# Kernel tuning notes

Measured on AMD Instinct MI355X. Metric: run time of the kernel, lower is better.

The kernel has to match this reference:

```python
import jax, jax.numpy as jnp
import numpy as np

H = 128
NC, NM, ND = 50000, 30000, 10000
E_CM, E_MD, E_CD = 800000, 400000, 800000


def setup_inputs() -> dict:
    key = jax.random.key(0)
    ks = jax.random.split(key, 20)
    nrm = lambda k, s: jax.random.normal(k, s, dtype=jnp.float32)
    ri = lambda k, n, hi: jax.random.randint(k, (n,), 0, hi, dtype=jnp.int32)
    scale = 1.0 / np.sqrt(H)
    return {
        'x_c': nrm(ks[0], (NC, H)),
        'x_m': nrm(ks[1], (NM, H)),
        'x_d': nrm(ks[2], (ND, H)),
        'src_cm': ri(ks[3], E_CM, NC), 'dst_cm': ri(ks[4], E_CM, NM),
        'src_md': ri(ks[5], E_MD, NM), 'dst_md': ri(ks[6], E_MD, ND),
        'src_cd': ri(ks[7], E_CD, NC), 'dst_cd': ri(ks[8], E_CD, ND),
        'src_mc': ri(ks[9], E_CM, NM), 'dst_mc': ri(ks[10], E_CM, NC),
        'src_dm': ri(ks[11], E_MD, ND), 'dst_dm': ri(ks[12], E_MD, NM),
        'src_dc': ri(ks[13], E_CD, ND), 'dst_dc': ri(ks[14], E_CD, NC),
        'Wl': nrm(ks[15], (4, 6, H, H)) * scale,  # lin_l per (layer, relation)
        'Wr': nrm(ks[16], (4, 6, H, H)) * scale,  # lin_r (root) per (layer, relation)
        'b': nrm(ks[17], (4, 6, H)) * scale,      # lin_l bias
    }


def _segment_mean(feat, seg, n):
    s = jax.ops.segment_sum(feat, seg, num_segments=n)
    cnt = jax.ops.segment_sum(jnp.ones((seg.shape[0], 1), feat.dtype), seg, num_segments=n)
    return s / jnp.maximum(cnt, 1.0)


def reference(x_c, x_m, x_d,
              src_cm, dst_cm, src_md, dst_md, src_cd, dst_cd,
              src_mc, dst_mc, src_dm, dst_dm, src_dc, dst_dc,
              Wl, Wr, b):
    # relation order: (c->m), (m->d), (c->d), (m->c), (d->m), (d->c)
    rels = [(src_cm, dst_cm, 'c', 'm', NM), (src_md, dst_md, 'm', 'd', ND),
            (src_cd, dst_cd, 'c', 'd', ND), (src_mc, dst_mc, 'm', 'c', NC),
            (src_dm, dst_dm, 'd', 'm', NM), (src_dc, dst_dc, 'd', 'c', NC)]

    def layer(h, l):
        outs = []
        for r, (s, dst, st, dt, nd) in enumerate(rels):
            agg = _segment_mean(h[st][s], dst, nd)          # gather + scatter-mean
            outs.append(agg @ Wl[l, r] + h[dt] @ Wr[l, r] + b[l, r])
        # HeteroConv aggr='mean': each dst type receives exactly 2 relations
        return {'c': (outs[3] + outs[5]) * 0.5,
                'm': (outs[0] + outs[4]) * 0.5,
                'd': (outs[1] + outs[2]) * 0.5}

    h = {'c': x_c, 'm': x_m, 'd': x_d}
    for l in range(3):
        h = layer(h, l)
        h = {k: jax.nn.relu(v) for k, v in h.items()}  # dropout is identity in eval
    h = layer(h, 3)

    def l2n(v):
        return v / jnp.maximum(jnp.linalg.norm(v, axis=1, keepdims=True), 1e-12)

    return (l2n(h['c']), l2n(h['m']), l2n(h['d']))
```

## Files before the change

### kernel.cpp

```cpp
#include <hip/hip_runtime.h>
#include <hip/hip_bf16.h>


#define NC_N 50000
#define NM_N 30000
#define ND_N 10000
#define NTOT 90000
#define H    128

typedef __attribute__((ext_vector_type(8))) short short8;
typedef __attribute__((ext_vector_type(4))) float f32x4;

__device__ __forceinline__ ushort f2bf(float f) {
    uint u = __float_as_uint(f);
    return (ushort)((u + 0x7fffu + ((u >> 16) & 1u)) >> 16);
}
__device__ __forceinline__ float bflo(uint v) { return __uint_as_float(v << 16); }
__device__ __forceinline__ float bfhi(uint v) { return __uint_as_float(v & 0xffff0000u); }

#define ACHUNK 2048

struct BuildArgs {
    const int* dstp[6];
    const int* srcp[6];
    int ablockBase[7];
    int binBase[7];
    int E[6];
    int offsBase[6];
    int csrBase[6];
    int nDst[6];
    int shift[6];
};

__global__ __launch_bounds__(256)
void bincount_k(BuildArgs a, int* __restrict__ binCnt) {
    __shared__ int hist[128];
    int blk = blockIdx.x, r = 0;
    #pragma unroll
    for (int k = 1; k <= 5; ++k) if (blk >= a.ablockBase[k]) r = k;
    const int i0 = (blk - a.ablockBase[r]) * ACHUNK;
    const int E = a.E[r], sh = a.shift[r];
    const int tid = threadIdx.x;
    if (tid < 128) hist[tid] = 0;
    __syncthreads();
    #pragma unroll
    for (int k = 0; k < 8; ++k) {
        int i = i0 + k * 256 + tid;
        if (i < E) atomicAdd(&hist[a.dstp[r][i] >> sh], 1);
    }
    __syncthreads();
    if (tid < 128 && hist[tid] > 0)
        atomicAdd(&binCnt[a.binBase[r] + tid], hist[tid]);
}

__global__ void binscan_k(const int* __restrict__ binCnt, int* __restrict__ binOffs,
                          int* __restrict__ binCur, int totBins) {
    __shared__ int buf[1024];
    int tid = threadIdx.x;
    int v = (tid < totBins) ? binCnt[tid] : 0;
    buf[tid] = v;
    __syncthreads();
    #pragma unroll
    for (int off = 1; off < 1024; off <<= 1) {
        int t = (tid >= off) ? buf[tid - off] : 0;
        __syncthreads();
        buf[tid] += t;
        __syncthreads();
    }
    if (tid < totBins) {
        int excl = buf[tid] - v;
        binOffs[tid] = excl;
        binCur[tid]  = excl;
        if (tid == totBins - 1) binOffs[totBins] = buf[tid];
    }
}

__global__ __launch_bounds__(256)
void binscat_k(BuildArgs a, int* __restrict__ binCur, int2* __restrict__ staging) {
    __shared__ int hist[128], hbase[128], hcur[128];
    int blk = blockIdx.x, r = 0;
    #pragma unroll
    for (int k = 1; k <= 5; ++k) if (blk >= a.ablockBase[k]) r = k;
    const int i0 = (blk - a.ablockBase[r]) * ACHUNK;
    const int E = a.E[r], sh = a.shift[r];
    const int tid = threadIdx.x;
    if (tid < 128) { hist[tid] = 0; hcur[tid] = 0; }
    __syncthreads();
    int d[8], s[8], bn[8];
    bool ok[8];
    #pragma unroll
    for (int k = 0; k < 8; ++k) {
        int i = i0 + k * 256 + tid;
        ok[k] = (i < E);
        if (ok[k]) {
            d[k] = a.dstp[r][i];
            s[k] = a.srcp[r][i];
            bn[k] = d[k] >> sh;
            atomicAdd(&hist[bn[k]], 1);
        }
    }
    __syncthreads();
    if (tid < 128 && hist[tid] > 0)
        hbase[tid] = atomicAdd(&binCur[a.binBase[r] + tid], hist[tid]);
    __syncthreads();
    #pragma unroll
    for (int k = 0; k < 8; ++k) {
        if (ok[k]) {
            int lr = atomicAdd(&hcur[bn[k]], 1);
            staging[hbase[bn[k]] + lr] = make_int2(s[k], d[k]);
        }
    }
}

__global__ __launch_bounds__(256)
void binplace2_k(BuildArgs a, const int* __restrict__ binOffs,
                 const int2* __restrict__ staging,
                 int* __restrict__ offsAll, int* __restrict__ csr) {
    __shared__ int cnt[512];
    __shared__ int sbuf[512];
    int g = blockIdx.x, r = 0;
    #pragma unroll
    for (int k = 1; k <= 5; ++k) if (g >= a.binBase[k]) r = k;
    const int b = g - a.binBase[r];
    const int sh = a.shift[r];
    const int dlo = b << sh;
    const int dhi = min(dlo + (1 << sh), a.nDst[r]);
    const int nd = dhi - dlo;
    const int tid = threadIdx.x;
    const int i0 = tid, i1 = tid + 256;
    cnt[i0] = 0; cnt[i1] = 0;
    __syncthreads();
    const int eBase = binOffs[g];
    const int eEnd  = binOffs[g + 1];
    for (int i = eBase + tid; i < eEnd; i += 256)
        atomicAdd(&cnt[staging[i].y - dlo], 1);
    __syncthreads();
    sbuf[i0] = cnt[i0]; sbuf[i1] = cnt[i1];
    __syncthreads();
    #pragma unroll
    for (int off = 1; off < 512; off <<= 1) {
        int t0 = (i0 >= off) ? sbuf[i0 - off] : 0;
        int t1 = (i1 >= off) ? sbuf[i1 - off] : 0;
        __syncthreads();
        sbuf[i0] += t0; sbuf[i1] += t1;
        __syncthreads();
    }
    const int eRel = eBase - a.csrBase[r];
    int e0 = sbuf[i0] - cnt[i0];
    int e1 = sbuf[i1] - cnt[i1];
    if (i0 < nd) { offsAll[a.offsBase[r] + dlo + i0] = eRel + e0; cnt[i0] = eBase + e0; }
    if (i1 < nd) { offsAll[a.offsBase[r] + dlo + i1] = eRel + e1; cnt[i1] = eBase + e1; }
    if (tid == 0 && dhi == a.nDst[r])
        offsAll[a.offsBase[r] + a.nDst[r]] = eRel + (eEnd - eBase);
    __syncthreads();
    for (int i = eBase + tid; i < eEnd; i += 256) {
        int2 p = staging[i];
        int pos = atomicAdd(&cnt[p.y - dlo], 1);
        csr[pos] = p.x;
    }
}

__global__ void prep_w_k(const float* __restrict__ Wl, const float* __restrict__ Wr,
                         const float* __restrict__ b,
                         ushort* __restrict__ WlT, ushort* __restrict__ WsumT,
                         float* __restrict__ bsum) {
    const int rA[3] = {3, 0, 1}, rB[3] = {5, 4, 2};
    int blk = blockIdx.x, tid = threadIdx.x;
    int nr = tid >> 1;
    int k0 = (tid & 1) * 64;
    if (blk < 24) {
        const float* src = Wl + (size_t)blk * 16384;
        ushort* dst = WlT + (size_t)blk * 16384;
        for (int k = k0; k < k0 + 64; ++k)
            dst[nr * 128 + k] = f2bf(src[k * 128 + nr]);
    } else {
        int lt = blk - 24, l = lt / 3, t = lt % 3;
        const float* sA = Wr + (size_t)(l * 6 + rA[t]) * 16384;
        const float* sB = Wr + (size_t)(l * 6 + rB[t]) * 16384;
        ushort* dst = WsumT + (size_t)lt * 16384;
        for (int k = k0; k < k0 + 64; ++k)
            dst[nr * 128 + k] = f2bf(sA[k * 128 + nr] + sB[k * 128 + nr]);
        if (tid < 128)
            bsum[lt * 128 + tid] = b[(l * 6 + rA[t]) * 128 + tid] +
                                   b[(l * 6 + rB[t]) * 128 + tid];
    }
}

__global__ void cvt_x_k(const float* __restrict__ xc, const float* __restrict__ xm,
                        const float* __restrict__ xd, ushort* __restrict__ h) {
    int i = blockIdx.x * 256 + threadIdx.x;
    const int tot = NTOT * H / 8;
    if (i >= tot) return;
    size_t base = (size_t)i * 8;
    int row = (int)(base >> 7);
    const float* src; size_t local;
    if (row < NC_N) { src = xc; local = base; }
    else if (row < NC_N + NM_N) { src = xm; local = base - (size_t)NC_N * H; }
    else { src = xd; local = base - (size_t)(NC_N + NM_N) * H; }
    float4 v0 = *(const float4*)(src + local);
    float4 v1 = *(const float4*)(src + local + 4);
    uint4 o;
    o.x = (uint)f2bf(v0.x) | ((uint)f2bf(v0.y) << 16);
    o.y = (uint)f2bf(v0.z) | ((uint)f2bf(v0.w) << 16);
    o.z = (uint)f2bf(v1.x) | ((uint)f2bf(v1.y) << 16);
    o.w = (uint)f2bf(v1.z) | ((uint)f2bf(v1.w) << 16);
    *(uint4*)(h + base) = o;
}

struct AggArgs {
    const ushort* src[6];
    const int* offs[6];
    const int* csr[6];
    ushort* out[6];
    int n[3];
    int blockBase[4];
    int halfBlocks[3];
};

__global__ __launch_bounds__(256)
void agg_all_k(AggArgs ga) {
    const int b = blockIdx.x;
    const int t = (b >= ga.blockBase[2]) ? 2 : (b >= ga.blockBase[1]) ? 1 : 0;
    const int local = b - ga.blockBase[t];
    const int isB = (local >= ga.halfBlocks[t]) ? 1 : 0;
    const int ridx = 2 * t + isB;
    const uint2* __restrict__ src = (const uint2*)ga.src[ridx];
    const int* __restrict__ offs  = ga.offs[ridx];
    const int* __restrict__ csr   = ga.csr[ridx];
    uint2* __restrict__ out       = (uint2*)ga.out[ridx];
    const int n = ga.n[t];
    const int w = (local - isB * ga.halfBlocks[t]) * 4 + (int)(threadIdx.x >> 6);
    if (w >= n) return;
    const int lane = threadIdx.x & 63;
    const int half = lane >> 5;
    const int lh   = lane & 31;
    const int s = offs[w], e = offs[w + 1];

    float a0 = 0.f, a1 = 0.f, a2 = 0.f, a3 = 0.f;
    int j = s;
    for (; j + 16 <= e; j += 16) {
        int i0 = csr[j + 0  + half], i1 = csr[j + 2  + half];
        int i2 = csr[j + 4  + half], i3 = csr[j + 6  + half];
        int i4 = csr[j + 8  + half], i5 = csr[j + 10 + half];
        int i6 = csr[j + 12 + half], i7 = csr[j + 14 + half];
        uint2 v0 = src[(size_t)i0 * 32 + lh];
        uint2 v1 = src[(size_t)i1 * 32 + lh];
        uint2 v2 = src[(size_t)i2 * 32 + lh];
        uint2 v3 = src[(size_t)i3 * 32 + lh];
        uint2 v4 = src[(size_t)i4 * 32 + lh];
        uint2 v5 = src[(size_t)i5 * 32 + lh];
        uint2 v6 = src[(size_t)i6 * 32 + lh];
        uint2 v7 = src[(size_t)i7 * 32 + lh];
        a0 += bflo(v0.x) + bflo(v1.x) + bflo(v2.x) + bflo(v3.x)
            + bflo(v4.x) + bflo(v5.x) + bflo(v6.x) + bflo(v7.x);
        a1 += bfhi(v0.x) + bfhi(v1.x) + bfhi(v2.x) + bfhi(v3.x)
            + bfhi(v4.x) + bfhi(v5.x) + bfhi(v6.x) + bfhi(v7.x);
        a2 += bflo(v0.y) + bflo(v1.y) + bflo(v2.y) + bflo(v3.y)
            + bflo(v4.y) + bflo(v5.y) + bflo(v6.y) + bflo(v7.y);
        a3 += bfhi(v0.y) + bfhi(v1.y) + bfhi(v2.y) + bfhi(v3.y)
            + bfhi(v4.y) + bfhi(v5.y) + bfhi(v6.y) + bfhi(v7.y);
    }
    for (; j + 2 <= e; j += 2) {
        int i0 = csr[j + half];
        uint2 v = src[(size_t)i0 * 32 + lh];
        a0 += bflo(v.x); a1 += bfhi(v.x); a2 += bflo(v.y); a3 += bfhi(v.y);
    }
    if (j < e && half == 0) {
        int i0 = csr[j];
        uint2 v = src[(size_t)i0 * 32 + lh];
        a0 += bflo(v.x); a1 += bfhi(v.x); a2 += bflo(v.y); a3 += bfhi(v.y);
    }
    a0 += __shfl_xor(a0, 32);
    a1 += __shfl_xor(a1, 32);
    a2 += __shfl_xor(a2, 32);
    a3 += __shfl_xor(a3, 32);
    if (half == 0) {
        const float inv = 1.0f / fmaxf((float)(e - s), 1.0f);
        uint2 o;
        o.x = (uint)f2bf(a0 * inv) | ((uint)f2bf(a1 * inv) << 16);
        o.y = (uint)f2bf(a2 * inv) | ((uint)f2bf(a3 * inv) << 16);
        out[(size_t)w * 32 + lh] = o;
    }
}

struct GemmArgs {
    const ushort* A1[3]; const ushort* W1[3];
    const ushort* A2[3]; const ushort* W2[3];
    const ushort* A3[3]; const ushort* W3[3];
    const float* bias[3];
    void* out[3];
    int n[3];
    int blockBase[4];
    int mode;
};

__global__ __launch_bounds__(256)
void gemm_all_k(GemmArgs ga) {
    __shared__ ushort As[128][40];
    __shared__ ushort Bs[128][40];
    const int b = blockIdx.x;
    const int t = (b >= ga.blockBase[2]) ? 2 : (b >= ga.blockBase[1]) ? 1 : 0;
    const int tid  = threadIdx.x;
    const int wave = tid >> 6, lane = tid & 63;
    const int lr = lane & 15, lk = lane >> 4;
    const int row0 = (b - ga.blockBase[t]) * 128;
    const int n = ga.n[t];

    f32x4 acc[2][8];
    #pragma unroll
    for (int i = 0; i < 2; ++i)
        #pragma unroll
        for (int j = 0; j < 8; ++j) acc[i][j] = (f32x4)0.f;

    const ushort* Ap[3] = {ga.A1[t], ga.A2[t], ga.A3[t]};
    const ushort* Wp[3] = {ga.W1[t], ga.W2[t], ga.W3[t]};

    const int rs = tid >> 2;
    const int kb = (tid & 3) * 8;

    for (int term = 0; term < 3; ++term) {
        const ushort* A = Ap[term];
        const ushort* W = Wp[term];
        #pragma unroll 1
        for (int k0 = 0; k0 < 128; k0 += 32) {
            #pragma unroll
            for (int p = 0; p < 2; ++p) {
                int rr = rs + p * 64;
                int gr = row0 + rr;
                short8 av = (short8)0;
                if (gr < n) av = *(const short8*)(A + (size_t)gr * 128 + k0 + kb);
                *(short8*)&As[rr][kb] = av;
                short8 wv = *(const short8*)(W + (size_t)rr * 128 + k0 + kb);
                *(short8*)&Bs[rr][kb] = wv;
            }
            __syncthreads();
            short8 af0 = *(const short8*)&As[wave * 32 + lr][lk * 8];
            short8 af1 = *(const short8*)&As[wave * 32 + 16 + lr][lk * 8];
            #pragma unroll
            for (int nt = 0; nt < 8; ++nt) {
                short8 bf = *(const short8*)&Bs[nt * 16 + lr][lk * 8];
                acc[0][nt] = __builtin_amdgcn_mfma_f32_16x16x32_bf16(af0, bf, acc[0][nt], 0, 0, 0);
                acc[1][nt] = __builtin_amdgcn_mfma_f32_16x16x32_bf16(af1, bf, acc[1][nt], 0, 0, 0);
            }
            __syncthreads();
        }
    }
    float bv[8];
    #pragma unroll
    for (int nt = 0; nt < 8; ++nt) bv[nt] = ga.bias[t][nt * 16 + lr];

    if (ga.mode == 0) {
        ushort* outp = (ushort*)ga.out[t];
        #pragma unroll
        for (int mt = 0; mt < 2; ++mt) {
            #pragma unroll
            for (int nt = 0; nt < 8; ++nt) {
                int col = nt * 16 + lr;
                #pragma unroll
                for (int r = 0; r < 4; ++r) {
                    int row = row0 + wave * 32 + mt * 16 + lk * 4 + r;
                    if (row < n) {
                        float v = fmaxf(0.5f * (acc[mt][nt][r] + bv[nt]), 0.f);
                        outp[(size_t)row * 128 + col] = f2bf(v);
                    }
                }
            }
        }
    } else {
        float* outp = (float*)ga.out[t];
        #pragma unroll
        for (int mt = 0; mt < 2; ++mt) {
            #pragma unroll
            for (int r = 0; r < 4; ++r) {
                float v[8]; float ss = 0.f;
                #pragma unroll
                for (int nt = 0; nt < 8; ++nt) {
                    v[nt] = 0.5f * (acc[mt][nt][r] + bv[nt]);
                    ss += v[nt] * v[nt];
                }
                ss += __shfl_xor(ss, 1);
                ss += __shfl_xor(ss, 2);
                ss += __shfl_xor(ss, 4);
                ss += __shfl_xor(ss, 8);
                float scale = 1.0f / fmaxf(sqrtf(ss), 1e-12f);
                int row = row0 + wave * 32 + mt * 16 + lk * 4 + r;
                if (row < n) {
                    #pragma unroll
                    for (int nt = 0; nt < 8; ++nt)
                        outp[(size_t)row * 128 + nt * 16 + lr] = v[nt] * scale;
                }
            }
        }
    }
}

extern "C" void kernel_launch(void* const* d_in, const int* in_sizes, int n_in,
                              void* d_out, int out_size, void* d_ws, size_t ws_size,
                              hipStream_t stream) {
    const float* x[3] = {(const float*)d_in[0], (const float*)d_in[1], (const float*)d_in[2]};
    const int* srcp[6] = {(const int*)d_in[3], (const int*)d_in[5], (const int*)d_in[7],
                          (const int*)d_in[9], (const int*)d_in[11], (const int*)d_in[13]};
    const int* dstp[6] = {(const int*)d_in[4], (const int*)d_in[6], (const int*)d_in[8],
                          (const int*)d_in[10], (const int*)d_in[12], (const int*)d_in[14]};
    const float* Wl = (const float*)d_in[15];
    const float* Wr = (const float*)d_in[16];
    const float* b  = (const float*)d_in[17];
    float* outp = (float*)d_out;

    const int nNode[3]   = {NC_N, NM_N, ND_N};
    const int E[6]       = {800000, 400000, 800000, 800000, 400000, 800000};
    const int nDst[6]    = {NM_N, ND_N, ND_N, NC_N, NM_N, NC_N};
    const int shiftR[6]  = {8, 7, 7, 9, 8, 9};
    const int srcType[6] = {0, 1, 0, 1, 2, 2};
    const int relA[3] = {3, 0, 1}, relB[3] = {5, 4, 2};

    char* p = (char*)d_ws;
    auto alloc = [&](size_t bytes) -> char* {
        char* r = p; p += (bytes + 255) & ~(size_t)255; return r;
    };
    ushort* hA    = (ushort*)alloc((size_t)NTOT * H * 2);
    ushort* hB    = (ushort*)alloc((size_t)NTOT * H * 2);
    ushort* aggA[3], * aggB[3];
    for (int t = 0; t < 3; ++t) {
        aggA[t] = (ushort*)alloc((size_t)nNode[t] * H * 2);
        aggB[t] = (ushort*)alloc((size_t)nNode[t] * H * 2);
    }
    ushort* WlT   = (ushort*)alloc((size_t)24 * H * H * 2);
    ushort* WsumT = (ushort*)alloc((size_t)12 * H * H * 2);
    float*  bsum  = (float*)alloc((size_t)12 * H * 4);
    int*    offs  = (int*)alloc((size_t)180006 * 4);
    int*    csr   = (int*)alloc((size_t)4000000 * 4);
    int*    binCnt  = (int*)alloc((size_t)1024 * 4);
    int*    binOffs = (int*)alloc((size_t)1025 * 4);
    int*    binCur  = (int*)alloc((size_t)1024 * 4);
    int2*   staging = (int2*)hA;

    BuildArgs ba;
    int totBins = 0;
    { int ob = 0, cb = 0, ab = 0, gb = 0;
      for (int r = 0; r < 6; ++r) {
          ba.dstp[r] = dstp[r]; ba.srcp[r] = srcp[r];
          ba.E[r] = E[r]; ba.nDst[r] = nDst[r]; ba.shift[r] = shiftR[r];
          ba.ablockBase[r] = ab; ab += (E[r] + ACHUNK - 1) / ACHUNK;
          ba.binBase[r]    = gb; gb += (nDst[r] + (1 << shiftR[r]) - 1) >> shiftR[r];
          ba.offsBase[r] = ob; ob += nDst[r] + 1;
          ba.csrBase[r]  = cb; cb += E[r];
      }
      ba.ablockBase[6] = ab; ba.binBase[6] = gb;
      totBins = gb; }

    hipMemsetAsync(binCnt, 0, totBins * 4, stream);
    bincount_k<<<ba.ablockBase[6], 256, 0, stream>>>(ba, binCnt);
    binscan_k<<<1, 1024, 0, stream>>>(binCnt, binOffs, binCur, totBins);
    binscat_k<<<ba.ablockBase[6], 256, 0, stream>>>(ba, binCur, staging);
    binplace2_k<<<totBins, 256, 0, stream>>>(ba, binOffs, staging, offs, csr);

    prep_w_k<<<36, 256, 0, stream>>>(Wl, Wr, b, WlT, WsumT, bsum);
    cvt_x_k<<<(NTOT * H / 8 + 255) / 256, 256, 0, stream>>>(x[0], x[1], x[2], hA);

    const size_t tOff[3] = {0, (size_t)NC_N * H, (size_t)(NC_N + NM_N) * H};
    ushort* hb[2] = {hA, hB};

    int cur = 0;
    for (int l = 0; l < 4; ++l) {
        ushort* hsrc = hb[cur];
        ushort* hdst = hb[cur ^ 1];

        AggArgs aa;
        int aggBlocks = 0;
        for (int t = 0; t < 3; ++t) {
            int rA = relA[t], rB = relB[t];
            aa.src[2 * t]     = hsrc + tOff[srcType[rA]];
            aa.offs[2 * t]    = offs + ba.offsBase[rA];
            aa.csr[2 * t]     = csr + ba.csrBase[rA];
            aa.out[2 * t]     = aggA[t];
            aa.src[2 * t + 1] = hsrc + tOff[srcType[rB]];
            aa.offs[2 * t + 1]= offs + ba.offsBase[rB];
            aa.csr[2 * t + 1] = csr + ba.csrBase[rB];
            aa.out[2 * t + 1] = aggB[t];
            aa.n[t] = nNode[t];
            aa.halfBlocks[t] = (nNode[t] + 3) / 4;
            aa.blockBase[t] = aggBlocks;
            aggBlocks += 2 * aa.halfBlocks[t];
        }
        aa.blockBase[3] = aggBlocks;
        agg_all_k<<<aggBlocks, 256, 0, stream>>>(aa);

        GemmArgs ga;
        int gemmBlocks = 0;
        for (int t = 0; t < 3; ++t) {
            int rA = relA[t], rB = relB[t];
            ga.A1[t] = aggA[t]; ga.W1[t] = WlT + (size_t)(l * 6 + rA) * H * H;
            ga.A2[t] = aggB[t]; ga.W2[t] = WlT + (size_t)(l * 6 + rB) * H * H;
            ga.A3[t] = hsrc + tOff[t];
            ga.W3[t] = WsumT + (size_t)(l * 3 + t) * H * H;
            ga.bias[t] = bsum + (size_t)(l * 3 + t) * H;
            ga.out[t] = (l < 3) ? (void*)(hdst + tOff[t]) : (void*)(outp + tOff[t]);
            ga.n[t] = nNode[t];
            ga.blockBase[t] = gemmBlocks;
            gemmBlocks += (nNode[t] + 127) / 128;
        }
        ga.blockBase[3] = gemmBlocks;
        ga.mode = (l < 3) ? 0 : 1;
        gemm_all_k<<<gemmBlocks, 256, 0, stream>>>(ga);

        cur ^= 1;
    }
}
```

Measured before the change: 877.0 us.

## Pad CSR adjacency rows to multiples of 16 with zero-row sentinel

The CSR build now pads each destination's neighbor list to a multiple of 16 entries, filling the extra slots with an index pointing at an all-zero row appended to the feature buffers. The aggregation kernel then runs only its fully unrolled 16-wide gather loop, with no tail loops. This removes the low-parallelism remainder iterations and their divergence. In exchange it adds redundant gathers of the zero row, a larger CSR array, and a second scan in the build.

```diff
diff --git a/kernel.cpp b/kernel.cpp
--- a/kernel.cpp
+++ b/kernel.cpp
@@ -7,6 +7,7 @@
 #define ND_N 10000
 #define NTOT 90000
 #define H    128
+#define PADG 16
 
 typedef __attribute__((ext_vector_type(8))) short short8;
 typedef __attribute__((ext_vector_type(4))) float f32x4;
@@ -30,6 +31,8 @@
     int csrBase[6];
     int nDst[6];
     int shift[6];
+    int padBase[6];
+    int zIdx[6];
 };
 
 __global__ __launch_bounds__(256)
@@ -115,7 +118,8 @@
 __global__ __launch_bounds__(256)
 void binplace2_k(BuildArgs a, const int* __restrict__ binOffs,
                  const int2* __restrict__ staging,
-                 int* __restrict__ offsAll, int* __restrict__ csr) {
+                 int* __restrict__ offsAll, int* __restrict__ poffsAll,
+                 int* __restrict__ csr) {
     __shared__ int cnt[512];
     __shared__ int sbuf[512];
     int g = blockIdx.x, r = 0;
@@ -135,7 +139,8 @@
     for (int i = eBase + tid; i < eEnd; i += 256)
         atomicAdd(&cnt[staging[i].y - dlo], 1);
     __syncthreads();
-    sbuf[i0] = cnt[i0]; sbuf[i1] = cnt[i1];
+    const int c0 = cnt[i0], c1 = cnt[i1];
+    sbuf[i0] = c0; sbuf[i1] = c1;
     __syncthreads();
     #pragma unroll
     for (int off = 1; off < 512; off <<= 1) {
@@ -145,18 +150,43 @@
         sbuf[i0] += t0; sbuf[i1] += t1;
         __syncthreads();
     }
+    const int rawe0 = sbuf[i0] - c0, rawe1 = sbuf[i1] - c1;
+    const int p0c = (c0 + PADG - 1) & ~(PADG - 1);
+    const int p1c = (c1 + PADG - 1) & ~(PADG - 1);
+    sbuf[i0] = p0c; sbuf[i1] = p1c;
+    __syncthreads();
+    #pragma unroll
+    for (int off = 1; off < 512; off <<= 1) {
+        int t0 = (i0 >= off) ? sbuf[i0 - off] : 0;
+        int t1 = (i1 >= off) ? sbuf[i1 - off] : 0;
+        __syncthreads();
+        sbuf[i0] += t0; sbuf[i1] += t1;
+        __syncthreads();
+    }
+    const int pe0 = sbuf[i0] - p0c, pe1 = sbuf[i1] - p1c;
     const int eRel = eBase - a.csrBase[r];
-    int e0 = sbuf[i0] - cnt[i0];
-    int e1 = sbuf[i1] - cnt[i1];
-    if (i0 < nd) { offsAll[a.offsBase[r] + dlo + i0] = eRel + e0; cnt[i0] = eBase + e0; }
-    if (i1 < nd) { offsAll[a.offsBase[r] + dlo + i1] = eRel + e1; cnt[i1] = eBase + e1; }
+    const int pBin = eBase + a.padBase[r] + b * ((1 << sh) * (PADG - 1));
+    const int zI = a.zIdx[r];
+    if (i0 < nd) {
+        offsAll[a.offsBase[r] + dlo + i0]  = eRel + rawe0;
+        poffsAll[a.offsBase[r] + dlo + i0] = pBin + pe0;
+        for (int k = c0; k < p0c; ++k) csr[pBin + pe0 + k] = zI;
+    }
+    if (i1 < nd) {
+        offsAll[a.offsBase[r] + dlo + i1]  = eRel + rawe1;
+        poffsAll[a.offsBase[r] + dlo + i1] = pBin + pe1;
+        for (int k = c1; k < p1c; ++k) csr[pBin + pe1 + k] = zI;
+    }
     if (tid == 0 && dhi == a.nDst[r])
         offsAll[a.offsBase[r] + a.nDst[r]] = eRel + (eEnd - eBase);
     __syncthreads();
+    if (i0 < nd) cnt[i0] = pBin + pe0;
+    if (i1 < nd) cnt[i1] = pBin + pe1;
+    __syncthreads();
     for (int i = eBase + tid; i < eEnd; i += 256) {
-        int2 p = staging[i];
-        int pos = atomicAdd(&cnt[p.y - dlo], 1);
-        csr[pos] = p.x;
+        int2 pv = staging[i];
+        int pos = atomicAdd(&cnt[pv.y - dlo], 1);
+        csr[pos] = pv.x;
     }
 }
 
@@ -210,7 +240,7 @@
 struct AggArgs {
     const ushort* src[6];
     const int* offs[6];
-    const int* csr[6];
+    const int* poffs[6];
     ushort* out[6];
     int n[3];
     int blockBase[4];
@@ -218,7 +248,7 @@
 };
 
 __global__ __launch_bounds__(256)
-void agg_all_k(AggArgs ga) {
+void agg_all_k(AggArgs ga, const int* __restrict__ csr) {
     const int b = blockIdx.x;
     const int t = (b >= ga.blockBase[2]) ? 2 : (b >= ga.blockBase[1]) ? 1 : 0;
     const int local = b - ga.blockBase[t];
@@ -226,7 +256,7 @@
     const int ridx = 2 * t + isB;
     const uint2* __restrict__ src = (const uint2*)ga.src[ridx];
     const int* __restrict__ offs  = ga.offs[ridx];
-    const int* __restrict__ csr   = ga.csr[ridx];
+    const int* __restrict__ poffs = ga.poffs[ridx];
     uint2* __restrict__ out       = (uint2*)ga.out[ridx];
     const int n = ga.n[t];
     const int w = (local - isB * ga.halfBlocks[t]) * 4 + (int)(threadIdx.x >> 6);
@@ -234,11 +264,12 @@
     const int lane = threadIdx.x & 63;
     const int half = lane >> 5;
     const int lh   = lane & 31;
-    const int s = offs[w], e = offs[w + 1];
+    const int deg  = offs[w + 1] - offs[w];
+    const int ps   = poffs[w];
+    const int pe   = ps + ((deg + PADG - 1) & ~(PADG - 1));
 
     float a0 = 0.f, a1 = 0.f, a2 = 0.f, a3 = 0.f;
-    int j = s;
-    for (; j + 16 <= e; j += 16) {
+    for (int j = ps; j < pe; j += 16) {
         int i0 = csr[j + 0  + half], i1 = csr[j + 2  + half];
         int i2 = csr[j + 4  + half], i3 = csr[j + 6  + half];
         int i4 = csr[j + 8  + half], i5 = csr[j + 10 + half];
@@ -260,22 +291,12 @@
         a3 += bfhi(v0.y) + bfhi(v1.y) + bfhi(v2.y) + bfhi(v3.y)
             + bfhi(v4.y) + bfhi(v5.y) + bfhi(v6.y) + bfhi(v7.y);
     }
-    for (; j + 2 <= e; j += 2) {
-        int i0 = csr[j + half];
-        uint2 v = src[(size_t)i0 * 32 + lh];
-        a0 += bflo(v.x); a1 += bfhi(v.x); a2 += bflo(v.y); a3 += bfhi(v.y);
-    }
-    if (j < e && half == 0) {
-        int i0 = csr[j];
-        uint2 v = src[(size_t)i0 * 32 + lh];
-        a0 += bflo(v.x); a1 += bfhi(v.x); a2 += bflo(v.y); a3 += bfhi(v.y);
-    }
     a0 += __shfl_xor(a0, 32);
     a1 += __shfl_xor(a1, 32);
     a2 += __shfl_xor(a2, 32);
     a3 += __shfl_xor(a3, 32);
     if (half == 0) {
-        const float inv = 1.0f / fmaxf((float)(e - s), 1.0f);
+        const float inv = 1.0f / fmaxf((float)deg, 1.0f);
         uint2 o;
         o.x = (uint)f2bf(a0 * inv) | ((uint)f2bf(a1 * inv) << 16);
         o.y = (uint)f2bf(a2 * inv) | ((uint)f2bf(a3 * inv) << 16);
@@ -413,13 +434,14 @@
     const int shiftR[6]  = {8, 7, 7, 9, 8, 9};
     const int srcType[6] = {0, 1, 0, 1, 2, 2};
     const int relA[3] = {3, 0, 1}, relB[3] = {5, 4, 2};
+    const int srcRowOff[3] = {0, NC_N, NC_N + NM_N};
 
     char* p = (char*)d_ws;
     auto alloc = [&](size_t bytes) -> char* {
         char* r = p; p += (bytes + 255) & ~(size_t)255; return r;
     };
-    ushort* hA    = (ushort*)alloc((size_t)NTOT * H * 2);
-    ushort* hB    = (ushort*)alloc((size_t)NTOT * H * 2);
+    ushort* hA    = (ushort*)alloc((size_t)(NTOT + 1) * H * 2);
+    ushort* hB    = (ushort*)alloc((size_t)(NTOT + 1) * H * 2);
     ushort* aggA[3], * aggB[3];
     for (int t = 0; t < 3; ++t) {
         aggA[t] = (ushort*)alloc((size_t)nNode[t] * H * 2);
@@ -429,32 +451,38 @@
     ushort* WsumT = (ushort*)alloc((size_t)12 * H * H * 2);
     float*  bsum  = (float*)alloc((size_t)12 * H * 4);
     int*    offs  = (int*)alloc((size_t)180006 * 4);
-    int*    csr   = (int*)alloc((size_t)4000000 * 4);
+    int*    poffs = (int*)alloc((size_t)180006 * 4);
     int*    binCnt  = (int*)alloc((size_t)1024 * 4);
     int*    binOffs = (int*)alloc((size_t)1025 * 4);
     int*    binCur  = (int*)alloc((size_t)1024 * 4);
     int2*   staging = (int2*)hA;
 
     BuildArgs ba;
-    int totBins = 0;
-    { int ob = 0, cb = 0, ab = 0, gb = 0;
+    int totBins = 0, padTot = 0;
+    { int ob = 0, cb = 0, ab = 0, gb = 0, pb = 0;
       for (int r = 0; r < 6; ++r) {
           ba.dstp[r] = dstp[r]; ba.srcp[r] = srcp[r];
           ba.E[r] = E[r]; ba.nDst[r] = nDst[r]; ba.shift[r] = shiftR[r];
+          ba.zIdx[r] = NTOT - srcRowOff[srcType[r]];
           ba.ablockBase[r] = ab; ab += (E[r] + ACHUNK - 1) / ACHUNK;
-          ba.binBase[r]    = gb; gb += (nDst[r] + (1 << shiftR[r]) - 1) >> shiftR[r];
+          int nb = (nDst[r] + (1 << shiftR[r]) - 1) >> shiftR[r];
+          ba.binBase[r] = gb; gb += nb;
           ba.offsBase[r] = ob; ob += nDst[r] + 1;
           ba.csrBase[r]  = cb; cb += E[r];
+          ba.padBase[r]  = pb; pb += nb * (1 << shiftR[r]) * (PADG - 1);
       }
       ba.ablockBase[6] = ab; ba.binBase[6] = gb;
-      totBins = gb; }
+      totBins = gb; padTot = pb; }
+    int* csr = (int*)alloc((size_t)(4000000 + padTot) * 4);
 
     hipMemsetAsync(binCnt, 0, totBins * 4, stream);
     bincount_k<<<ba.ablockBase[6], 256, 0, stream>>>(ba, binCnt);
     binscan_k<<<1, 1024, 0, stream>>>(binCnt, binOffs, binCur, totBins);
     binscat_k<<<ba.ablockBase[6], 256, 0, stream>>>(ba, binCur, staging);
-    binplace2_k<<<totBins, 256, 0, stream>>>(ba, binOffs, staging, offs, csr);
-
+    binplace2_k<<<totBins, 256, 0, stream>>>(ba, binOffs, staging, offs, poffs, csr);
+
+    hipMemsetAsync(hA + (size_t)NTOT * H, 0, H * 2, stream);
+    hipMemsetAsync(hB + (size_t)NTOT * H, 0, H * 2, stream);
     prep_w_k<<<36, 256, 0, stream>>>(Wl, Wr, b, WlT, WsumT, bsum);
     cvt_x_k<<<(NTOT * H / 8 + 255) / 256, 256, 0, stream>>>(x[0], x[1], x[2], hA);
 
@@ -470,21 +498,21 @@
         int aggBlocks = 0;
         for (int t = 0; t < 3; ++t) {
             int rA = relA[t], rB = relB[t];
-            aa.src[2 * t]     = hsrc + tOff[srcType[rA]];
-            aa.offs[2 * t]    = offs + ba.offsBase[rA];
-            aa.csr[2 * t]     = csr + ba.csrBase[rA];
-            aa.out[2 * t]     = aggA[t];
-            aa.src[2 * t + 1] = hsrc + tOff[srcType[rB]];
-            aa.offs[2 * t + 1]= offs + ba.offsBase[rB];
-            aa.csr[2 * t + 1] = csr + ba.csrBase[rB];
-            aa.out[2 * t + 1] = aggB[t];
+            aa.src[2 * t]      = hsrc + tOff[srcType[rA]];
+            aa.offs[2 * t]     = offs + ba.offsBase[rA];
+            aa.poffs[2 * t]    = poffs + ba.offsBase[rA];
+            aa.out[2 * t]      = aggA[t];
+            aa.src[2 * t + 1]  = hsrc + tOff[srcType[rB]];
+            aa.offs[2 * t + 1] = offs + ba.offsBase[rB];
+            aa.poffs[2 * t + 1]= poffs + ba.offsBase[rB];
+            aa.out[2 * t + 1]  = aggB[t];
             aa.n[t] = nNode[t];
             aa.halfBlocks[t] = (nNode[t] + 3) / 4;
             aa.blockBase[t] = aggBlocks;
             aggBlocks += 2 * aa.halfBlocks[t];
         }
         aa.blockBase[3] = aggBlocks;
-        agg_all_k<<<aggBlocks, 256, 0, stream>>>(aa);
+        agg_all_k<<<aggBlocks, 256, 0, stream>>>(aa, csr);
 
         GemmArgs ga;
         int gemmBlocks = 0;
```

After: 835.1 us. 4.8% less time.
